# Kernel optimization log

Hardware: AMD Instinct MI355X
Metric: run time of the kernel (lower is better)

## Reference

```python
import jax, jax.numpy as jnp
import numpy as np

N_NODES = 50000
N_EDGES = 800000
D_IN = 96
D_OUT = 96


def setup_inputs() -> dict:
    key = jax.random.key(0)
    k1, k2, k3 = jax.random.split(key, 3)
    x = jax.random.normal(k1, (N_NODES, D_IN), dtype=jnp.float32)
    edge_index = jax.random.randint(k2, (2, N_EDGES), 0, N_NODES, dtype=jnp.int64)
    edge_weight = jnp.ones((N_EDGES,), dtype=jnp.float32)
    # Glorot-ish init for the linear weight, zero bias (as in PyG GCNConv)
    W = jax.random.normal(k3, (D_IN, D_OUT), dtype=jnp.float32) * (1.0 / np.sqrt(D_IN))
    b = jnp.zeros((D_OUT,), dtype=jnp.float32)
    return {"x": x, "edge_index": edge_index, "edge_weight": edge_weight, "W": W, "b": b}


def reference(x, edge_index, edge_weight, W, b):
    """PyG GCNConv: out = D^{-1/2} (A + I) D^{-1/2} (x @ W) + b."""
    N = x.shape[0]
    row, col = edge_index[0], edge_index[1]  # source -> target
    # add self loops with weight 1 (PyG default add_self_loops=True)
    loop = jnp.arange(N, dtype=edge_index.dtype)
    row = jnp.concatenate([row, loop])
    col = jnp.concatenate([col, loop])
    ew = jnp.concatenate([edge_weight, jnp.ones((N,), dtype=edge_weight.dtype)])
    # symmetric normalization based on (weighted) in-degree over col
    deg = jax.ops.segment_sum(ew, col, num_segments=N)  # [N]
    dinv = jnp.where(deg > 0, jax.lax.rsqrt(deg), 0.0)
    norm = dinv[row] * ew * dinv[col]  # [E+N]
    # linear transform first (small GEMM), then gather-scale-scatter over edges
    h = x @ W  # [N, D_OUT]
    msg = h[row] * norm[:, None]  # [E+N, D_OUT]
    out = jax.ops.segment_sum(msg, col, num_segments=N)  # [N, D_OUT]
    return out + b
```

## Files before the change

### kernel.cpp

```cpp
#include <hip/hip_runtime.h>

#define N_NODES 50000
#define N_EDGES 800000
#define D 96
#define NBKT 512
#define BNODES 98
#define BCAP 2304
#define PART_B 250
#define EPB 3200
#define EPT 13
#define CAP 48
#define NSLOT (BNODES * CAP)
#define GEMM_B 782
#define NTILE 21
#define GCAP (NTILE * CAP)
#define GATHER_B ((N_NODES + NTILE - 1) / NTILE)

typedef float vfloat4 __attribute__((ext_vector_type(4)));

__device__ __forceinline__ float bf_lo(unsigned u) { return __uint_as_float(u << 16); }
__device__ __forceinline__ float bf_hi(unsigned u) { return __uint_as_float(u & 0xFFFF0000u); }
__device__ __forceinline__ unsigned f2bf_bits(unsigned u) {
    return (u + 0x7FFFu + ((u >> 16) & 1u)) & 0xFFFF0000u;
}
__device__ __forceinline__ unsigned pack_bf2(float a, float b) {
    return (f2bf_bits(__float_as_uint(a)) >> 16) | f2bf_bits(__float_as_uint(b));
}

__device__ __forceinline__ int exscan256(int v, int* wsum) {
    int lane = threadIdx.x & 63;
    int wave = threadIdx.x >> 6;
    int incl = v;
#pragma unroll
    for (int off = 1; off < 64; off <<= 1) {
        int t = __shfl_up(incl, off);
        if (lane >= off) incl += t;
    }
    if (lane == 63) wsum[wave] = incl;
    __syncthreads();
    int base = 0;
#pragma unroll
    for (int wv = 0; wv < 3; ++wv) base += (wv < wave) ? wsum[wv] : 0;
    return base + incl - v;
}

__global__ __launch_bounds__(256) void k_part(const int* __restrict__ row,
                                              const int* __restrict__ col,
                                              const float* __restrict__ ew,
                                              int* __restrict__ bkt_cnt,
                                              uint2* __restrict__ bktbuf) {
    __shared__ int hist[NBKT];
    __shared__ int cur[NBKT];
    int tid = threadIdx.x;
    hist[tid] = 0;
    hist[tid + 256] = 0;
    __syncthreads();
    int e0 = blockIdx.x * EPB;
    int myc[EPT];
#pragma unroll
    for (int k = 0; k < EPT; ++k) {
        int i = tid + 256 * k;
        myc[k] = (i < EPB) ? col[e0 + i] : -1;
    }
#pragma unroll
    for (int k = 0; k < EPT; ++k)
        if (myc[k] >= 0) atomicAdd(&hist[myc[k] / BNODES], 1);
    __syncthreads();
    {
        int h0 = hist[tid], h1 = hist[tid + 256];
        cur[tid] = h0 ? atomicAdd(&bkt_cnt[tid], h0) : 0;
        cur[tid + 256] = h1 ? atomicAdd(&bkt_cnt[tid + 256], h1) : 0;
    }
    __syncthreads();
#pragma unroll
    for (int k = 0; k < EPT; ++k) {
        int i = tid + 256 * k;
        if (myc[k] >= 0) {
            int e = e0 + i;
            int c = myc[k];
            int b = c / BNODES;
            int p = atomicAdd(&cur[b], 1);
            if (p < BCAP)
                bktbuf[(size_t)b * BCAP + p] =
                    make_uint2((unsigned)row[e] | ((unsigned)(c - b * BNODES) << 16),
                               __float_as_uint(ew[e]));
        }
    }
}

__global__ __launch_bounds__(256) void k_bingemm(
    const int* __restrict__ bkt_cnt, const uint2* __restrict__ bktbuf,
    const float* __restrict__ x, const float* __restrict__ W,
    unsigned* __restrict__ recs, int* __restrict__ rowptr,
    float* __restrict__ dinv, unsigned short* __restrict__ hb) {
    __shared__ int wsum1[4];
    __shared__ int wsum2[4];
    __shared__ int sbkt[NBKT];
    __shared__ int lcnt[BNODES];
    __shared__ int loff[256];
    __shared__ unsigned lslot[NSLOT];
    int tid = threadIdx.x;
    int bid = blockIdx.x;

    if (bid < NBKT) {
        int b = bid;
        int c0 = min(bkt_cnt[2 * tid], BCAP);
        int c1 = min(bkt_cnt[2 * tid + 1], BCAP);
        int ps = exscan256(c0 + c1, wsum1);
        sbkt[2 * tid] = ps;
        sbkt[2 * tid + 1] = ps + c0;
        if (tid < BNODES) lcnt[tid] = 0;
        __syncthreads();
        int gbase = sbkt[b];
        int ne = min(bkt_cnt[b], BCAP);

        for (int i = tid; i < ne; i += 256) {
            uint2 r = bktbuf[(size_t)b * BCAP + i];
            int lc = (int)(r.x >> 16);
            int p = atomicAdd(&lcnt[lc], 1);
            if (p < CAP) lslot[lc * CAP + p] = f2bf_bits(r.y) | (r.x & 0xFFFFu);
        }
        __syncthreads();

        int myv = (tid < BNODES) ? min(lcnt[tid], CAP) : 0;
        int ex2 = exscan256(myv, wsum2);
        loff[tid] = ex2;
        __syncthreads();

        for (int i = tid; i < NSLOT; i += 256) {
            int ln = i / CAP, s = i % CAP;
            if (s < min(lcnt[ln], CAP))
                recs[gbase + loff[ln] + s] = lslot[i];
        }
        int base = b * BNODES;
        if (tid < BNODES) {
            int n = base + tid;
            if (n <= N_NODES) rowptr[n] = gbase + loff[tid];
            if (n < N_NODES) {
                int cn = min(lcnt[tid], CAP);
                float d = 1.0f;
                for (int k = 0; k < cn; ++k) d += bf_hi(lslot[tid * CAP + k]);
                dinv[n] = rsqrtf(d);
            }
        }
    } else {
        int g = bid - NBKT;
        int lane = tid & 63;
        int j0 = __builtin_amdgcn_readfirstlane((tid >> 6) * 24);
        int n = g * 64 + lane;
        bool act = (n < N_NODES);
        const float* xr = x + (size_t)(act ? n : 0) * D;

        float acc[24] = {};
        for (int k4 = 0; k4 < D / 4; ++k4) {
            float4 xv = *(const float4*)&xr[k4 * 4];
#pragma unroll
            for (int kk = 0; kk < 4; ++kk) {
                float xs = (kk == 0) ? xv.x : (kk == 1) ? xv.y
                         : (kk == 2) ? xv.z : xv.w;
                const float* Wr = W + (k4 * 4 + kk) * D + j0;
#pragma unroll
                for (int jj = 0; jj < 24; ++jj)
                    acc[jj] += xs * Wr[jj];
            }
        }
        if (act) {
            unsigned short* hp = hb + (size_t)n * D + j0;
            uint4 u0, u1, u2;
            u0.x = pack_bf2(acc[0], acc[1]);   u0.y = pack_bf2(acc[2], acc[3]);
            u0.z = pack_bf2(acc[4], acc[5]);   u0.w = pack_bf2(acc[6], acc[7]);
            u1.x = pack_bf2(acc[8], acc[9]);   u1.y = pack_bf2(acc[10], acc[11]);
            u1.z = pack_bf2(acc[12], acc[13]); u1.w = pack_bf2(acc[14], acc[15]);
            u2.x = pack_bf2(acc[16], acc[17]); u2.y = pack_bf2(acc[18], acc[19]);
            u2.z = pack_bf2(acc[20], acc[21]); u2.w = pack_bf2(acc[22], acc[23]);
            *(uint4*)(hp) = u0;
            *(uint4*)(hp + 8) = u1;
            *(uint4*)(hp + 16) = u2;
        }
    }
}

__global__ __launch_bounds__(256) void k_gather(const int* __restrict__ rowptr,
                                                const unsigned* __restrict__ recs,
                                                const unsigned short* __restrict__ hb,
                                                const float* __restrict__ dinv,
                                                const float* __restrict__ bias,
                                                float* __restrict__ out) {
    __shared__ uint2 sed[GCAP];
    __shared__ int sptr[NTILE + 1];
    __shared__ unsigned char perm[NTILE];
    int tid = threadIdx.x;
    int nb = blockIdx.x * NTILE;

    if (tid <= NTILE) sptr[tid] = rowptr[min(nb + tid, N_NODES)];
    __syncthreads();
    if (tid < NTILE) {
        int dmy = sptr[tid + 1] - sptr[tid];
        int rank = 0;
#pragma unroll
        for (int jn = 0; jn < NTILE; ++jn) {
            int dj = sptr[jn + 1] - sptr[jn];
            rank += (dj > dmy) || (dj == dmy && jn < tid);
        }
        perm[rank] = (unsigned char)tid;
    }
    int e0 = sptr[0];
    int stage = sptr[NTILE] - e0;
    for (int i = tid; i < stage; i += 256) {
        unsigned r = recs[e0 + i];
        int src = (int)(r & 0xFFFFu);
        sed[i] = make_uint2((unsigned)src,
                            __float_as_uint(bf_hi(r) * dinv[src]));
    }
    __syncthreads();

    int lg = tid / 12;
    int jq = tid % 12;
    int pl = (lg < NTILE) ? perm[lg] : 0;
    int n = nb + pl;
    bool act = (lg < NTILE) && (n < N_NODES);
    int j = jq * 8;

    float di = act ? dinv[n] : 0.f;
    float acc[8] = {};
    if (act) {
        uint4 sv = *(const uint4*)(hb + (size_t)n * D + j);
        acc[0] = bf_lo(sv.x) * di; acc[1] = bf_hi(sv.x) * di;
        acc[2] = bf_lo(sv.y) * di; acc[3] = bf_hi(sv.y) * di;
        acc[4] = bf_lo(sv.z) * di; acc[5] = bf_hi(sv.z) * di;
        acc[6] = bf_lo(sv.w) * di; acc[7] = bf_hi(sv.w) * di;
    }

    int ls = act ? (sptr[pl] - e0) : 0;
    int le = act ? (sptr[pl + 1] - e0) : 0;
    int idx = ls;
    for (; idx + 4 <= le; idx += 4) {
        uint2 e0r = sed[idx], e1r = sed[idx + 1];
        uint2 e2r = sed[idx + 2], e3r = sed[idx + 3];
        uint4 v0 = *(const uint4*)(hb + (size_t)e0r.x * D + j);
        uint4 v1 = *(const uint4*)(hb + (size_t)e1r.x * D + j);
        uint4 v2 = *(const uint4*)(hb + (size_t)e2r.x * D + j);
        uint4 v3 = *(const uint4*)(hb + (size_t)e3r.x * D + j);
        float w0 = __uint_as_float(e0r.y), w1 = __uint_as_float(e1r.y);
        float w2 = __uint_as_float(e2r.y), w3 = __uint_as_float(e3r.y);
        acc[0] += w0 * bf_lo(v0.x); acc[1] += w0 * bf_hi(v0.x);
        acc[2] += w0 * bf_lo(v0.y); acc[3] += w0 * bf_hi(v0.y);
        acc[4] += w0 * bf_lo(v0.z); acc[5] += w0 * bf_hi(v0.z);
        acc[6] += w0 * bf_lo(v0.w); acc[7] += w0 * bf_hi(v0.w);
        acc[0] += w1 * bf_lo(v1.x); acc[1] += w1 * bf_hi(v1.x);
        acc[2] += w1 * bf_lo(v1.y); acc[3] += w1 * bf_hi(v1.y);
        acc[4] += w1 * bf_lo(v1.z); acc[5] += w1 * bf_hi(v1.z);
        acc[6] += w1 * bf_lo(v1.w); acc[7] += w1 * bf_hi(v1.w);
        acc[0] += w2 * bf_lo(v2.x); acc[1] += w2 * bf_hi(v2.x);
        acc[2] += w2 * bf_lo(v2.y); acc[3] += w2 * bf_hi(v2.y);
        acc[4] += w2 * bf_lo(v2.z); acc[5] += w2 * bf_hi(v2.z);
        acc[6] += w2 * bf_lo(v2.w); acc[7] += w2 * bf_hi(v2.w);
        acc[0] += w3 * bf_lo(v3.x); acc[1] += w3 * bf_hi(v3.x);
        acc[2] += w3 * bf_lo(v3.y); acc[3] += w3 * bf_hi(v3.y);
        acc[4] += w3 * bf_lo(v3.z); acc[5] += w3 * bf_hi(v3.z);
        acc[6] += w3 * bf_lo(v3.w); acc[7] += w3 * bf_hi(v3.w);
    }
    for (; idx < le; ++idx) {
        uint2 er = sed[idx];
        uint4 v0 = *(const uint4*)(hb + (size_t)er.x * D + j);
        float w0 = __uint_as_float(er.y);
        acc[0] += w0 * bf_lo(v0.x); acc[1] += w0 * bf_hi(v0.x);
        acc[2] += w0 * bf_lo(v0.y); acc[3] += w0 * bf_hi(v0.y);
        acc[4] += w0 * bf_lo(v0.z); acc[5] += w0 * bf_hi(v0.z);
        acc[6] += w0 * bf_lo(v0.w); acc[7] += w0 * bf_hi(v0.w);
    }

    if (act) {
        float4 b0 = *(const float4*)&bias[j];
        float4 b1 = *(const float4*)&bias[j + 4];
        vfloat4 o0, o1;
        o0.x = acc[0] * di + b0.x; o0.y = acc[1] * di + b0.y;
        o0.z = acc[2] * di + b0.z; o0.w = acc[3] * di + b0.w;
        o1.x = acc[4] * di + b1.x; o1.y = acc[5] * di + b1.y;
        o1.z = acc[6] * di + b1.z; o1.w = acc[7] * di + b1.w;
        __builtin_nontemporal_store(o0, (vfloat4*)&out[(size_t)n * D + j]);
        __builtin_nontemporal_store(o1, (vfloat4*)&out[(size_t)n * D + j + 4]);
    }
}

extern "C" void kernel_launch(void* const* d_in, const int* in_sizes, int n_in,
                              void* d_out, int out_size, void* d_ws, size_t ws_size,
                              hipStream_t stream) {
    const float* x  = (const float*)d_in[0];
    const int*   ei = (const int*)d_in[1];
    const float* ew = (const float*)d_in[2];
    const float* W  = (const float*)d_in[3];
    const float* b  = (const float*)d_in[4];
    float* out = (float*)d_out;

    const int* row = ei;
    const int* col = ei + N_EDGES;

    char* p = (char*)d_ws;
    unsigned short* hb     = (unsigned short*)p;   p += (size_t)N_NODES * D * 2;
    uint2*          bktbuf = (uint2*)p;            p += (size_t)NBKT * BCAP * 8;
    unsigned*       recs   = (unsigned*)p;         p += (size_t)N_EDGES * 4;
    int*            rowptr = (int*)p;              p += (size_t)(N_NODES + 64) * 4;
    float*          dinv   = (float*)p;            p += (size_t)N_NODES * 4;
    int*            bkt_cnt= (int*)p;              p += (size_t)NBKT * 4;

    (void)hipMemsetAsync(bkt_cnt, 0, NBKT * sizeof(int), stream);
    k_part   <<<PART_B, 256, 0, stream>>>(row, col, ew, bkt_cnt, bktbuf);
    k_bingemm<<<NBKT + GEMM_B, 256, 0, stream>>>(bkt_cnt, bktbuf, x, W,
                                                 recs, rowptr, dinv, hb);
    k_gather <<<GATHER_B, 256, 0, stream>>>(rowptr, recs, hb, dinv, b, out);
}
```

Baseline: 141.7 us.

## Split GEMM tiles between partition and binning kernels to balance load

Half of the x@W GEMM tiles now run alongside the edge-partition blocks in a merged first kernel, and the other half stay in the binning kernel. Independent GEMM work fills the GPU while the atomic-heavy partition step runs, and the second kernel gets shorter. The cost is a larger first launch whose GEMM blocks compete with partition blocks for bandwidth and CUs.

```diff
diff --git a/kernel.cpp b/kernel.cpp
--- a/kernel.cpp
+++ b/kernel.cpp
@@ -12,6 +12,7 @@
 #define CAP 48
 #define NSLOT (BNODES * CAP)
 #define GEMM_B 782
+#define GEMM_H 391
 #define NTILE 21
 #define GCAP (NTILE * CAP)
 #define GATHER_B ((N_NODES + NTILE - 1) / NTILE)
@@ -44,47 +45,92 @@
     return base + incl - v;
 }
 
-__global__ __launch_bounds__(256) void k_part(const int* __restrict__ row,
-                                              const int* __restrict__ col,
-                                              const float* __restrict__ ew,
-                                              int* __restrict__ bkt_cnt,
-                                              uint2* __restrict__ bktbuf) {
-    __shared__ int hist[NBKT];
-    __shared__ int cur[NBKT];
+__device__ __forceinline__ void gemm_tile(int g, int tid,
+                                          const float* __restrict__ x,
+                                          const float* __restrict__ W,
+                                          unsigned short* __restrict__ hb) {
+    int lane = tid & 63;
+    int j0 = __builtin_amdgcn_readfirstlane((tid >> 6) * 24);
+    int n = g * 64 + lane;
+    bool act = (n < N_NODES);
+    const float* xr = x + (size_t)(act ? n : 0) * D;
+
+    float acc[24] = {};
+    for (int k4 = 0; k4 < D / 4; ++k4) {
+        float4 xv = *(const float4*)&xr[k4 * 4];
+#pragma unroll
+        for (int kk = 0; kk < 4; ++kk) {
+            float xs = (kk == 0) ? xv.x : (kk == 1) ? xv.y
+                     : (kk == 2) ? xv.z : xv.w;
+            const float* Wr = W + (k4 * 4 + kk) * D + j0;
+#pragma unroll
+            for (int jj = 0; jj < 24; ++jj)
+                acc[jj] += xs * Wr[jj];
+        }
+    }
+    if (act) {
+        unsigned short* hp = hb + (size_t)n * D + j0;
+        uint4 u0, u1, u2;
+        u0.x = pack_bf2(acc[0], acc[1]);   u0.y = pack_bf2(acc[2], acc[3]);
+        u0.z = pack_bf2(acc[4], acc[5]);   u0.w = pack_bf2(acc[6], acc[7]);
+        u1.x = pack_bf2(acc[8], acc[9]);   u1.y = pack_bf2(acc[10], acc[11]);
+        u1.z = pack_bf2(acc[12], acc[13]); u1.w = pack_bf2(acc[14], acc[15]);
+        u2.x = pack_bf2(acc[16], acc[17]); u2.y = pack_bf2(acc[18], acc[19]);
+        u2.z = pack_bf2(acc[20], acc[21]); u2.w = pack_bf2(acc[22], acc[23]);
+        *(uint4*)(hp) = u0;
+        *(uint4*)(hp + 8) = u1;
+        *(uint4*)(hp + 16) = u2;
+    }
+}
+
+__global__ __launch_bounds__(256) void k_partgemm(
+    const int* __restrict__ row, const int* __restrict__ col,
+    const float* __restrict__ ew, const float* __restrict__ x,
+    const float* __restrict__ W, int* __restrict__ bkt_cnt,
+    uint2* __restrict__ bktbuf, unsigned short* __restrict__ hb) {
+    __shared__ int sh[2 * NBKT];
     int tid = threadIdx.x;
-    hist[tid] = 0;
-    hist[tid + 256] = 0;
-    __syncthreads();
-    int e0 = blockIdx.x * EPB;
-    int myc[EPT];
-#pragma unroll
-    for (int k = 0; k < EPT; ++k) {
-        int i = tid + 256 * k;
-        myc[k] = (i < EPB) ? col[e0 + i] : -1;
-    }
-#pragma unroll
-    for (int k = 0; k < EPT; ++k)
-        if (myc[k] >= 0) atomicAdd(&hist[myc[k] / BNODES], 1);
-    __syncthreads();
-    {
-        int h0 = hist[tid], h1 = hist[tid + 256];
-        cur[tid] = h0 ? atomicAdd(&bkt_cnt[tid], h0) : 0;
-        cur[tid + 256] = h1 ? atomicAdd(&bkt_cnt[tid + 256], h1) : 0;
-    }
-    __syncthreads();
-#pragma unroll
-    for (int k = 0; k < EPT; ++k) {
-        int i = tid + 256 * k;
-        if (myc[k] >= 0) {
-            int e = e0 + i;
-            int c = myc[k];
-            int b = c / BNODES;
-            int p = atomicAdd(&cur[b], 1);
-            if (p < BCAP)
-                bktbuf[(size_t)b * BCAP + p] =
-                    make_uint2((unsigned)row[e] | ((unsigned)(c - b * BNODES) << 16),
-                               __float_as_uint(ew[e]));
-        }
+    int bid = blockIdx.x;
+
+    if (bid < PART_B) {
+        int* hist = sh;
+        int* cur = sh + NBKT;
+        hist[tid] = 0;
+        hist[tid + 256] = 0;
+        __syncthreads();
+        int e0 = bid * EPB;
+        int myc[EPT];
+#pragma unroll
+        for (int k = 0; k < EPT; ++k) {
+            int i = tid + 256 * k;
+            myc[k] = (i < EPB) ? col[e0 + i] : -1;
+        }
+#pragma unroll
+        for (int k = 0; k < EPT; ++k)
+            if (myc[k] >= 0) atomicAdd(&hist[myc[k] / BNODES], 1);
+        __syncthreads();
+        {
+            int h0 = hist[tid], h1 = hist[tid + 256];
+            cur[tid] = h0 ? atomicAdd(&bkt_cnt[tid], h0) : 0;
+            cur[tid + 256] = h1 ? atomicAdd(&bkt_cnt[tid + 256], h1) : 0;
+        }
+        __syncthreads();
+#pragma unroll
+        for (int k = 0; k < EPT; ++k) {
+            int i = tid + 256 * k;
+            if (myc[k] >= 0) {
+                int e = e0 + i;
+                int c = myc[k];
+                int b = c / BNODES;
+                int p = atomicAdd(&cur[b], 1);
+                if (p < BCAP)
+                    bktbuf[(size_t)b * BCAP + p] =
+                        make_uint2((unsigned)row[e] | ((unsigned)(c - b * BNODES) << 16),
+                                   __float_as_uint(ew[e]));
+            }
+        }
+    } else {
+        gemm_tile(bid - PART_B, tid, x, W, hb);
     }
 }
 
@@ -144,39 +190,7 @@
             }
         }
     } else {
-        int g = bid - NBKT;
-        int lane = tid & 63;
-        int j0 = __builtin_amdgcn_readfirstlane((tid >> 6) * 24);
-        int n = g * 64 + lane;
-        bool act = (n < N_NODES);
-        const float* xr = x + (size_t)(act ? n : 0) * D;
-
-        float acc[24] = {};
-        for (int k4 = 0; k4 < D / 4; ++k4) {
-            float4 xv = *(const float4*)&xr[k4 * 4];
-#pragma unroll
-            for (int kk = 0; kk < 4; ++kk) {
-                float xs = (kk == 0) ? xv.x : (kk == 1) ? xv.y
-                         : (kk == 2) ? xv.z : xv.w;
-                const float* Wr = W + (k4 * 4 + kk) * D + j0;
-#pragma unroll
-                for (int jj = 0; jj < 24; ++jj)
-                    acc[jj] += xs * Wr[jj];
-            }
-        }
-        if (act) {
-            unsigned short* hp = hb + (size_t)n * D + j0;
-            uint4 u0, u1, u2;
-            u0.x = pack_bf2(acc[0], acc[1]);   u0.y = pack_bf2(acc[2], acc[3]);
-            u0.z = pack_bf2(acc[4], acc[5]);   u0.w = pack_bf2(acc[6], acc[7]);
-            u1.x = pack_bf2(acc[8], acc[9]);   u1.y = pack_bf2(acc[10], acc[11]);
-            u1.z = pack_bf2(acc[12], acc[13]); u1.w = pack_bf2(acc[14], acc[15]);
-            u2.x = pack_bf2(acc[16], acc[17]); u2.y = pack_bf2(acc[18], acc[19]);
-            u2.z = pack_bf2(acc[20], acc[21]); u2.w = pack_bf2(acc[22], acc[23]);
-            *(uint4*)(hp) = u0;
-            *(uint4*)(hp + 8) = u1;
-            *(uint4*)(hp + 16) = u2;
-        }
+        gemm_tile(bid - NBKT + GEMM_H, tid, x, W, hb);
     }
 }
 
@@ -305,8 +319,9 @@
     int*            bkt_cnt= (int*)p;              p += (size_t)NBKT * 4;
 
     (void)hipMemsetAsync(bkt_cnt, 0, NBKT * sizeof(int), stream);
-    k_part   <<<PART_B, 256, 0, stream>>>(row, col, ew, bkt_cnt, bktbuf);
-    k_bingemm<<<NBKT + GEMM_B, 256, 0, stream>>>(bkt_cnt, bktbuf, x, W,
-                                                 recs, rowptr, dinv, hb);
+    k_partgemm<<<PART_B + GEMM_H, 256, 0, stream>>>(row, col, ew, x, W,
+                                                    bkt_cnt, bktbuf, hb);
+    k_bingemm<<<NBKT + (GEMM_B - GEMM_H), 256, 0, stream>>>(bkt_cnt, bktbuf, x, W,
+                                                            recs, rowptr, dinv, hb);
     k_gather <<<GATHER_B, 256, 0, stream>>>(rowptr, recs, hb, dinv, b, out);
 }
```

After: 141.7 us. About the same (+0.0%).
